# Kernel optimization log

Measured on AMD Instinct MI355X. Metric: run time of the kernel, lower is better.

## Reference

```python
import jax, jax.numpy as jnp
from jax import lax
import numpy as np

EPS = 1e-5  # BatchNorm2d default eps

def _cbs(x, w, g, b, m, v, pad):
    # Conv2d(bias=False) + BatchNorm2d (eval mode, running stats) + SiLU
    y = lax.conv_general_dilated(x, w, (1, 1), [(pad, pad), (pad, pad)],
                                 dimension_numbers=('NCHW', 'OIHW', 'NCHW'))
    y = (y - m[None, :, None, None]) * (g / jnp.sqrt(v + EPS))[None, :, None, None] + b[None, :, None, None]
    return y * jax.nn.sigmoid(y)

def setup_inputs():
    key = jax.random.key(0)
    B, C1, C2, H, W = 2, 128, 128, 20, 20
    ks = iter(jax.random.split(key, 16))
    def wconv(o, i, s):
        return jax.random.normal(next(ks), (o, i, s, s), jnp.float32) / np.float32(np.sqrt(i * s * s))
    def bn(cdim):
        k1, k2 = jax.random.split(next(ks))
        g = jax.random.uniform(k1, (cdim,), jnp.float32, 0.5, 1.5)
        b = jax.random.normal(k2, (cdim,), jnp.float32) * 0.1
        return g, b, jnp.zeros((cdim,), jnp.float32), jnp.ones((cdim,), jnp.float32)
    inp = {'x': jax.random.normal(next(ks), (B, C1, H, W), jnp.float32)}
    inp['w1'] = wconv(C2, C1, 1); inp['g1'], inp['b1'], inp['m1'], inp['v1'] = bn(C2)
    inp['w2'] = wconv(C2, C1, 1); inp['g2'], inp['b2'], inp['m2'], inp['v2'] = bn(C2)
    inp['wr1'] = wconv(C2, 2 * C2, 1); inp['gr1'], inp['br1'], inp['mr1'], inp['vr1'] = bn(C2)
    inp['wr2'] = wconv(C2, C2, 3); inp['gr2'], inp['br2'], inp['mr2'], inp['vr2'] = bn(C2)
    inp['wr3'] = wconv(1, C2, 1); inp['gr3'], inp['br3'], inp['mr3'], inp['vr3'] = bn(1)
    return inp

def reference(x, w1, g1, b1, m1, v1, w2, g2, b2, m2, v2,
              wr1, gr1, br1, mr1, vr1, wr2, gr2, br2, mr2, vr2,
              wr3, gr3, br3, mr3, vr3):
    B, C, H, W = x.shape
    HW = H * W
    # feat: [B, HW, C2]
    feat = _cbs(x, w1, g1, b1, m1, v1, 0).reshape(B, -1, HW).transpose(0, 2, 1)
    C2 = feat.shape[-1]
    # pairwise concat: rel[b,i,j] = [feat[b,i], feat[b,j]]  -> [B, HW, HW, 2*C2]
    fi = jnp.broadcast_to(feat[:, :, None, :], (B, HW, HW, C2))
    fj = jnp.broadcast_to(feat[:, None, :, :], (B, HW, HW, C2))
    rel = jnp.concatenate([fi, fj], axis=-1)
    # faithful permute(0,3,1,2) + contiguous view to [B*HW, 2*C2, H, W]
    rel = rel.transpose(0, 3, 1, 2).reshape(B * HW, 2 * C2, H, W)
    r = _cbs(rel, wr1, gr1, br1, mr1, vr1, 0)
    r = _cbs(r, wr2, gr2, br2, mr2, vr2, 1)
    r = _cbs(r, wr3, gr3, br3, mr3, vr3, 0)  # [B*HW, 1, H, W]
    scores = r.reshape(B, HW, HW)
    # bmm aggregation then back to [B, C2, H, W]
    att = jnp.einsum('bij,bjc->bic', scores, feat).transpose(0, 2, 1).reshape(B, C2, H, W)
    return _cbs(att, w2, g2, b2, m2, v2, 0) + x
```

## Files before the change

### kernel.cpp

```cpp
#include <hip/hip_runtime.h>

#define EPS 1e-5f

typedef __bf16 bf16x8 __attribute__((ext_vector_type(8)));
typedef float  f32x4  __attribute__((ext_vector_type(4)));

__device__ __forceinline__ unsigned short f2bf(float f) {
  unsigned int u = __float_as_uint(f);
  unsigned int r = (u + 0x7fffu + ((u >> 16) & 1u)) >> 16;
  return (unsigned short)r;
}
__device__ __forceinline__ float silu(float y) {
  return y * __builtin_amdgcn_rcpf(1.f + __expf(-y));
}

__global__ void prep_kernel(const float* __restrict__ x, const float* __restrict__ w1,
                            const float* __restrict__ g1, const float* __restrict__ b1,
                            const float* __restrict__ m1, const float* __restrict__ v1,
                            const float* __restrict__ wr2, const float* __restrict__ wr1,
                            float* __restrict__ feat, float* __restrict__ featT,
                            float* __restrict__ attz,
                            unsigned short* __restrict__ Apack, float* __restrict__ Pfx,
                            float* __restrict__ Wt, float* __restrict__ wr1T) {
  int blk = blockIdx.x;
  int tid = threadIdx.x;
  if (blk < 400) {
    int hp = tid >> 7, c = tid & 127;
    int pp = blk * 2 + hp;
    int b = pp / 400, p = pp % 400;
    __shared__ float xv[2][128];
    xv[hp][c] = x[(b * 128 + c) * 400 + p];
    __syncthreads();
    const float4* w4 = (const float4*)(w1 + c * 128);
    const float4* v4 = (const float4*)xv[hp];
    float s0 = 0.f, s1 = 0.f, s2 = 0.f, s3 = 0.f;
#pragma unroll
    for (int i = 0; i < 32; ++i) {
      float4 wv = w4[i], xx = v4[i];
      s0 += wv.x * xx.x; s1 += wv.y * xx.y; s2 += wv.z * xx.z; s3 += wv.w * xx.w;
    }
    float s = (s0 + s1) + (s2 + s3);
    float sc = g1[c] * rsqrtf(v1[c] + EPS);
    float y = s * sc + (b1[c] - m1[c] * sc);
    float f = silu(y);
    feat[(b * 400 + p) * 128 + c] = f;
    featT[(b * 128 + c) * 400 + p] = f;
    if (p >= 200) attz[(b * 400 + p) * 128 + c] = 0.f;
  } else if (blk < 472) {
    int f = (blk - 400) * 4 + (tid >> 6);
    int lane = tid & 63;
    int tap = f >> 5, ks = (f >> 3) & 3, m8 = f & 7;
    int o  = m8 * 16 + (lane & 15);
    int cb = ks * 32 + (lane >> 4) * 8;
    unsigned short* dst = Apack + ((size_t)f * 64 + lane) * 8;
#pragma unroll
    for (int j = 0; j < 8; ++j)
      dst[j] = f2bf(wr2[(o * 128 + (cb + j)) * 9 + tap]);
  } else if (blk < 504) {
    int o = (blk - 472) * 4 + (tid >> 6);
    int lane = tid & 63;
    float4 wv = ((const float4*)(wr1 + o * 256))[lane];
    float p0 = wv.x, p1 = p0 + wv.y, p2 = p1 + wv.z, p3 = p2 + wv.w;
    float v = p3;
#pragma unroll
    for (int d = 1; d < 64; d <<= 1) {
      float t = __shfl_up(v, d);
      if (lane >= d) v += t;
    }
    float off = v - p3;
    float* Po = Pfx + o * 257;
    if (lane == 0) Po[0] = 0.f;
    Po[lane * 4 + 1] = off + p0;
    Po[lane * 4 + 2] = off + p1;
    Po[lane * 4 + 3] = off + p2;
    Po[lane * 4 + 4] = off + p3;
  } else if (blk < 648) {
    int base = (blk - 504) * 1024;
#pragma unroll
    for (int k = 0; k < 4; ++k) {
      int idx = base + k * 256 + tid;
      int tap = idx >> 14;
      int r = idx & 16383;
      int i = r >> 7, o = r & 127;
      Wt[idx] = wr2[(o * 128 + i) * 9 + tap];
    }
  } else {
    int base = (blk - 648) * 1024;
#pragma unroll
    for (int k = 0; k < 4; ++k) {
      int idx = base + k * 256 + tid;
      int i = idx >> 7, o = idx & 127;
      wr1T[idx] = wr1[o * 256 + i];
    }
  }
}

__global__ __launch_bounds__(512, 4) void rel_kernel(
    const float* __restrict__ feat, const float* __restrict__ featT,
    const float* __restrict__ wr1T, const float* __restrict__ Pfx,
    const float* __restrict__ gr1, const float* __restrict__ br1,
    const float* __restrict__ mr1, const float* __restrict__ vr1,
    const unsigned short* __restrict__ Apack, const float* __restrict__ Wt,
    const float* __restrict__ gr2, const float* __restrict__ br2,
    const float* __restrict__ mr2, const float* __restrict__ vr2,
    const float* __restrict__ wr3,
    const float* __restrict__ gr3, const float* __restrict__ br3,
    const float* __restrict__ mr3, const float* __restrict__ vr3,
    float* __restrict__ att) {

  __shared__ __align__(16) unsigned short r1f[16 * 221 * 8];
  __shared__ float f0s[220], f1s[220], scoreS[208];
  __shared__ float wB0s[128], wB1s[128];
  __shared__ float sc1[128], sh1[128], sc2[128], sh2[128], w3c[128];
  __shared__ float attT[128];
  __shared__ float fA[256], r1c[128], AvS[128];
  __shared__ float vS[9 * 128];
  __shared__ float spS[9];
  __shared__ float spP[400];

  int tid = threadIdx.x, lane = tid & 63, wid = tid >> 6;
  int blk = blockIdx.x;

  if (tid < 128) {
    float s1 = gr1[tid] * rsqrtf(vr1[tid] + EPS); sc1[tid] = s1; sh1[tid] = br1[tid] - mr1[tid] * s1;
    float s2 = gr2[tid] * rsqrtf(vr2[tid] + EPS); sc2[tid] = s2; sh2[tid] = br2[tid] - mr2[tid] * s2;
    w3c[tid] = wr3[tid];
    attT[tid] = 0.f; AvS[tid] = 0.f;
  }
  float s3 = gr3[0] * rsqrtf(vr3[0] + EPS);
  float sh3 = br3[0] - mr3[0] * s3;

  if (blk < 800) {
    int idx = blk >> 1, half = blk & 1;
    int b = idx / 200, q = 200 + idx % 200;
    int c0 = (q * 256) / 400, c1 = c0 + 1;
    if (tid < 128) {
      const float* Po = Pfx + tid * 257;
      int e0 = min(256, 400 * c0 + 400 - 256 * q);
      wB0s[tid] = Po[e0];
      float wv = 0.f;
      if (c1 < 256) {
        int s1i = min(256, max(0, 400 * c1 - 256 * q));
        wv = Po[256] - Po[s1i];
      }
      wB1s[tid] = wv;
    }
    if (tid < 220) {
      int p = tid + 180 * half;
      f0s[tid] = featT[(b * 128 + (c0 - 128)) * 400 + p];
      f1s[tid] = (c1 < 256) ? featT[(b * 128 + (c1 - 128)) * 400 + p] : 0.f;
    }
    if (tid < 208) scoreS[tid] = 0.f;
    __syncthreads();

    for (int i = tid; i < 3520; i += 512) {
      int plane = i / 220, p = i - plane * 220;
      int cb = (plane >> 2) * 32 + (plane & 3) * 8;
      float fa0 = f0s[p], fa1 = f1s[p];
      unsigned int pk[4];
#pragma unroll
      for (int jp = 0; jp < 4; ++jp) {
        int c = cb + jp * 2;
        float y0 = wB0s[c] * fa0 + wB1s[c] * fa1;     y0 = y0 * sc1[c] + sh1[c];
        float y1 = wB0s[c + 1] * fa0 + wB1s[c + 1] * fa1; y1 = y1 * sc1[c + 1] + sh1[c + 1];
        pk[jp] = (unsigned int)f2bf(silu(y0)) | ((unsigned int)f2bf(silu(y1)) << 16);
      }
      *(uint4*)&r1f[(plane * 221 + p) * 8] = make_uint4(pk[0], pk[1], pk[2], pk[3]);
    }
    if (tid < 16) *(uint4*)&r1f[(tid * 221 + 220) * 8] = make_uint4(0, 0, 0, 0);

    int wm = wid & 1, wn = wid >> 1;
    int ntcnt = (wn == 0) ? 4 : 3;
    int n16 = lane & 15, quad = lane >> 4;
    int hA[4], wA[4], poA[4]; bool pov[4];
#pragma unroll
    for (int t = 0; t < 4; ++t) {
      int po = (wn + 4 * t) * 16 + n16;
      poA[t] = po; pov[t] = po < 200;
      int pg = half * 200 + po;
      hA[t] = pg / 20; wA[t] = pg - 20 * hA[t];
    }
    f32x4 acc[4][4];
#pragma unroll
    for (int mt = 0; mt < 4; ++mt)
#pragma unroll
      for (int t = 0; t < 4; ++t) acc[mt][t] = f32x4{0.f, 0.f, 0.f, 0.f};

    __syncthreads();

    const char* wbase = (const char*)Apack + (size_t)((wm * 4) * 64 + lane) * 16;
    for (int tap = 0; tap < 9; ++tap) {
      int dy = tap / 3 - 1, dx = tap % 3 - 1;
      int pp[4];
#pragma unroll
      for (int t = 0; t < 4; ++t) {
        int hh = hA[t] + dy, ww = wA[t] + dx;
        bool valid = pov[t] & (hh >= 0) & (hh < 20) & (ww >= 0) & (ww < 20);
        pp[t] = valid ? (hh - 9 * half) * 20 + ww : 220;
      }
#pragma unroll
      for (int ks = 0; ks < 4; ++ks) {
        const char* wp = wbase + (size_t)(tap * 4 + ks) * 8192;
        bf16x8 af0 = *(const bf16x8*)(wp);
        bf16x8 af1 = *(const bf16x8*)(wp + 1024);
        bf16x8 af2 = *(const bf16x8*)(wp + 2048);
        bf16x8 af3 = *(const bf16x8*)(wp + 3072);
        int pbase = (ks * 4 + quad) * 221;
#pragma unroll
        for (int t = 0; t < 4; ++t) {
          if (t < ntcnt) {
            bf16x8 bfr = *(const bf16x8*)&r1f[(pbase + pp[t]) * 8];
            acc[0][t] = __builtin_amdgcn_mfma_f32_16x16x32_bf16(af0, bfr, acc[0][t], 0, 0, 0);
            acc[1][t] = __builtin_amdgcn_mfma_f32_16x16x32_bf16(af1, bfr, acc[1][t], 0, 0, 0);
            acc[2][t] = __builtin_amdgcn_mfma_f32_16x16x32_bf16(af2, bfr, acc[2][t], 0, 0, 0);
            acc[3][t] = __builtin_amdgcn_mfma_f32_16x16x32_bf16(af3, bfr, acc[3][t], 0, 0, 0);
          }
        }
      }
    }

#pragma unroll
    for (int t = 0; t < 4; ++t) {
      if (t < ntcnt) {
        float ps = 0.f;
#pragma unroll
        for (int mt = 0; mt < 4; ++mt) {
#pragma unroll
          for (int r = 0; r < 4; ++r) {
            int o = wm * 64 + mt * 16 + quad * 4 + r;
            float y = acc[mt][t][r] * sc2[o] + sh2[o];
            ps += silu(y) * w3c[o];
          }
        }
        ps += __shfl_xor(ps, 16);
        ps += __shfl_xor(ps, 32);
        if (quad == 0 && pov[t]) atomicAdd(&scoreS[poA[t]], ps);
      }
    }
    __syncthreads();

    if (tid < 200) scoreS[tid] = silu(scoreS[tid] * s3 + sh3);
    __syncthreads();

    {
      int c = tid & 127, part = tid >> 7;
      float s = 0.f;
      int j0 = part * 50;
      const float* fb = feat + ((size_t)(b * 400 + half * 200 + j0)) * 128 + c;
#pragma unroll 10
      for (int j = 0; j < 50; ++j)
        s += scoreS[j0 + j] * fb[(size_t)j * 128];
      atomicAdd(&attT[c], s);
    }
    __syncthreads();
    if (tid < 128)
      atomicAdd(&att[((size_t)(b * 400 + q)) * 128 + tid], attT[tid]);
  } else {
    int cidx = blk - 800;
    int b = cidx / 200, q = cidx % 200;
    if (tid < 256) {
      int u = q * 256 + tid; int c = u / 400, i2 = u - c * 400;
      fA[tid] = featT[(b * 128 + c) * 400 + i2];
    }
    for (int k = tid; k < 1152; k += 512) vS[k] = 0.f;
    __syncthreads();
    {
      int o = tid & 127, part = tid >> 7;
      const float* wt = wr1T + part * 64 * 128 + o;
      const float* fv = fA + part * 64;
      float a = 0.f;
#pragma unroll 8
      for (int k = 0; k < 64; ++k) a += wt[k * 128] * fv[k];
      atomicAdd(&AvS[o], a);
    }
    __syncthreads();
    if (tid < 128) r1c[tid] = silu(AvS[tid] * sc1[tid] + sh1[tid]);
    __syncthreads();
    {
      int o = tid & 127, part = tid >> 7;
      const float* rc = r1c + part * 32;
      for (int tap = 0; tap < 9; ++tap) {
        const float* wt = Wt + tap * 16384 + part * 32 * 128 + o;
        float s = 0.f;
#pragma unroll 8
        for (int i2 = 0; i2 < 32; ++i2) s += wt[i2 * 128] * rc[i2];
        atomicAdd(&vS[tap * 128 + o], s);
      }
    }
    __syncthreads();
    for (int pat = wid; pat < 9; pat += 8) {
      int ry = pat / 3, rx = pat % 3;
      float ps = 0.f;
      for (int oo = lane; oo < 128; oo += 64) {
        float y = 0.f;
#pragma unroll
        for (int dy = -1; dy <= 1; ++dy) {
          if ((ry == 0 && dy < 0) || (ry == 2 && dy > 0)) continue;
#pragma unroll
          for (int dx = -1; dx <= 1; ++dx) {
            if ((rx == 0 && dx < 0) || (rx == 2 && dx > 0)) continue;
            y += vS[((dy + 1) * 3 + (dx + 1)) * 128 + oo];
          }
        }
        y = y * sc2[oo] + sh2[oo];
        ps += silu(y) * w3c[oo];
      }
#pragma unroll
      for (int sft = 32; sft >= 1; sft >>= 1) ps += __shfl_xor(ps, sft);
      if (lane == 0) spS[pat] = silu(ps * s3 + sh3);
    }
    __syncthreads();

    for (int p = tid; p < 400; p += 512) {
      int r = p / 20, cm = p - 20 * r;
      int ry = (r == 0) ? 0 : (r == 19) ? 2 : 1;
      int rx = (cm == 0) ? 0 : (cm == 19) ? 2 : 1;
      spP[p] = spS[ry * 3 + rx];
    }
    __syncthreads();
    {
      int c = tid & 127, part = tid >> 7;
      const float* fb = feat + ((size_t)(b * 400) + part * 100) * 128 + c;
      const float* sp = spP + part * 100;
      float s = 0.f;
#pragma unroll 10
      for (int j = 0; j < 100; ++j) s += sp[j] * fb[(size_t)j * 128];
      atomicAdd(&attT[c], s);
    }
    __syncthreads();
    if (tid < 128)
      att[((size_t)(b * 400 + q)) * 128 + tid] = attT[tid];
  }
}

__global__ void out_kernel(const float* __restrict__ att, const float* __restrict__ x,
                           const float* __restrict__ w2,
                           const float* __restrict__ g2, const float* __restrict__ b2,
                           const float* __restrict__ m2, const float* __restrict__ v2,
                           float* __restrict__ out) {
  int pp = blockIdx.x;
  int b = pp / 400, p = pp % 400;
  int tid = threadIdx.x;
  __shared__ float av[128];
  if (tid < 128) av[tid] = att[(size_t)(b * 400 + p) * 128 + tid];
  __syncthreads();
  int c = tid >> 1, part = tid & 1;
  const float4* w4 = (const float4*)(w2 + c * 128 + part * 64);
  const float4* v4 = (const float4*)(av + part * 64);
  float s0 = 0.f, s1 = 0.f, s2 = 0.f, s3 = 0.f;
#pragma unroll
  for (int i = 0; i < 16; ++i) {
    float4 wv = w4[i], xx = v4[i];
    s0 += wv.x * xx.x; s1 += wv.y * xx.y; s2 += wv.z * xx.z; s3 += wv.w * xx.w;
  }
  float s = (s0 + s1) + (s2 + s3);
  s += __shfl_xor(s, 1);
  if (part == 0) {
    float sc = g2[c] * rsqrtf(v2[c] + EPS);
    float y = s * sc + (b2[c] - m2[c] * sc);
    int xi = (b * 128 + c) * 400 + p;
    out[xi] = silu(y) + x[xi];
  }
}

extern "C" void kernel_launch(void* const* d_in, const int* in_sizes, int n_in,
                              void* d_out, int out_size, void* d_ws, size_t ws_size,
                              hipStream_t stream) {
  const float* x   = (const float*)d_in[0];
  const float* w1  = (const float*)d_in[1];
  const float* g1  = (const float*)d_in[2];
  const float* b1  = (const float*)d_in[3];
  const float* m1  = (const float*)d_in[4];
  const float* v1  = (const float*)d_in[5];
  const float* w2  = (const float*)d_in[6];
  const float* g2  = (const float*)d_in[7];
  const float* b2  = (const float*)d_in[8];
  const float* m2  = (const float*)d_in[9];
  const float* v2  = (const float*)d_in[10];
  const float* wr1 = (const float*)d_in[11];
  const float* gr1 = (const float*)d_in[12];
  const float* br1 = (const float*)d_in[13];
  const float* mr1 = (const float*)d_in[14];
  const float* vr1 = (const float*)d_in[15];
  const float* wr2 = (const float*)d_in[16];
  const float* gr2 = (const float*)d_in[17];
  const float* br2 = (const float*)d_in[18];
  const float* mr2 = (const float*)d_in[19];
  const float* vr2 = (const float*)d_in[20];
  const float* wr3 = (const float*)d_in[21];
  const float* gr3 = (const float*)d_in[22];
  const float* br3 = (const float*)d_in[23];
  const float* mr3 = (const float*)d_in[24];
  const float* vr3 = (const float*)d_in[25];
  float* out = (float*)d_out;

  char* ws = (char*)d_ws;
  float*          feat  = (float*)ws;
  float*          attb  = (float*)(ws + 409600);
  unsigned short* Apack = (unsigned short*)(ws + 819200);
  float*          Pfx   = (float*)(ws + 1114112);
  float*          Wt    = (float*)(ws + 1245696);
  float*          featT = (float*)(ws + 1901056);
  float*          wr1T  = (float*)(ws + 2310656);

  prep_kernel<<<680, 256, 0, stream>>>(x, w1, g1, b1, m1, v1, wr2, wr1,
                                       feat, featT, attb, Apack, Pfx, Wt, wr1T);
  rel_kernel<<<1200, 512, 0, stream>>>(feat, featT, wr1T, Pfx, gr1, br1, mr1, vr1,
                                       Apack, Wt,
                                       gr2, br2, mr2, vr2, wr3, gr3, br3, mr3, vr3, attb);
  out_kernel<<<800, 256, 0, stream>>>(attb, x, w2, g2, b2, m2, v2, out);
}
```

Measured before the change: 205.2 us.

## Fuse output conv into rel kernel using last-block completion counters

Drops the separate out_kernel. The final 1x1 conv, BN, SiLU and residual add now run inside rel_kernel. For the pair-split rows, a per-row atomic counter (zeroed in prep_kernel) picks the second finishing block, which reads the accumulated att row and writes the output. The single-block rows compute the output straight from shared memory. This removes one kernel launch and a global round-trip of att, at the cost of a threadfence, an extra atomic and a serialized tail in some blocks. The counter buffer reuses workspace rows that are no longer written.

```diff
diff --git a/kernel.cpp b/kernel.cpp
--- a/kernel.cpp
+++ b/kernel.cpp
@@ -19,7 +19,7 @@
                             const float* __restrict__ m1, const float* __restrict__ v1,
                             const float* __restrict__ wr2, const float* __restrict__ wr1,
                             float* __restrict__ feat, float* __restrict__ featT,
-                            float* __restrict__ attz,
+                            float* __restrict__ attz, int* __restrict__ cnt,
                             unsigned short* __restrict__ Apack, float* __restrict__ Pfx,
                             float* __restrict__ Wt, float* __restrict__ wr1T) {
   int blk = blockIdx.x;
@@ -45,7 +45,10 @@
     float f = silu(y);
     feat[(b * 400 + p) * 128 + c] = f;
     featT[(b * 128 + c) * 400 + p] = f;
-    if (p >= 200) attz[(b * 400 + p) * 128 + c] = 0.f;
+    if (p >= 200) {
+      attz[(b * 400 + p) * 128 + c] = 0.f;
+      if (c == 0) cnt[b * 200 + (p - 200)] = 0;
+    }
   } else if (blk < 472) {
     int f = (blk - 400) * 4 + (tid >> 6);
     int lane = tid & 63;
@@ -106,17 +109,23 @@
     const float* __restrict__ wr3,
     const float* __restrict__ gr3, const float* __restrict__ br3,
     const float* __restrict__ mr3, const float* __restrict__ vr3,
-    float* __restrict__ att) {
+    float* __restrict__ att, int* __restrict__ cnt,
+    const float* __restrict__ x, const float* __restrict__ w2,
+    const float* __restrict__ g2, const float* __restrict__ b2,
+    const float* __restrict__ m2, const float* __restrict__ v2,
+    float* __restrict__ out) {
 
   __shared__ __align__(16) unsigned short r1f[16 * 221 * 8];
   __shared__ float f0s[220], f1s[220], scoreS[208];
   __shared__ float wB0s[128], wB1s[128];
   __shared__ float sc1[128], sh1[128], sc2[128], sh2[128], w3c[128];
-  __shared__ float attT[128];
-  __shared__ float fA[256], r1c[128], AvS[128];
+  __shared__ __align__(16) float attT[128];
+  __shared__ __align__(16) float fA[256];
+  __shared__ float r1c[128], AvS[128];
   __shared__ float vS[9 * 128];
   __shared__ float spS[9];
   __shared__ float spP[400];
+  __shared__ int lastFlag;
 
   int tid = threadIdx.x, lane = tid & 63, wid = tid >> 6;
   int blk = blockIdx.x;
@@ -255,6 +264,34 @@
     __syncthreads();
     if (tid < 128)
       atomicAdd(&att[((size_t)(b * 400 + q)) * 128 + tid], attT[tid]);
+    __threadfence();
+    __syncthreads();
+    if (tid == 0)
+      lastFlag = (atomicAdd(&cnt[b * 200 + (q - 200)], 1) == 1);
+    __syncthreads();
+    if (lastFlag) {
+      float* arow = att + ((size_t)(b * 400 + q)) * 128;
+      if (tid < 128) fA[tid] = atomicAdd(&arow[tid], 0.0f);
+      __syncthreads();
+      int c = tid >> 2, sub = tid & 3;
+      const float4* w4 = (const float4*)(w2 + c * 128 + sub * 32);
+      const float4* v4 = (const float4*)(fA + sub * 32);
+      float s0 = 0.f, s1 = 0.f, s2v = 0.f, s3v = 0.f;
+#pragma unroll
+      for (int i = 0; i < 8; ++i) {
+        float4 wv = w4[i], xx = v4[i];
+        s0 += wv.x * xx.x; s1 += wv.y * xx.y; s2v += wv.z * xx.z; s3v += wv.w * xx.w;
+      }
+      float s = (s0 + s1) + (s2v + s3v);
+      s += __shfl_xor(s, 1);
+      s += __shfl_xor(s, 2);
+      if (sub == 0) {
+        float scc = g2[c] * rsqrtf(v2[c] + EPS);
+        float y = s * scc + (b2[c] - m2[c] * scc);
+        int xi = (b * 128 + c) * 400 + q;
+        out[xi] = silu(y) + x[xi];
+      }
+    }
   } else {
     int cidx = blk - 800;
     int b = cidx / 200, q = cidx % 200;
@@ -328,38 +365,26 @@
       atomicAdd(&attT[c], s);
     }
     __syncthreads();
-    if (tid < 128)
-      att[((size_t)(b * 400 + q)) * 128 + tid] = attT[tid];
-  }
-}
-
-__global__ void out_kernel(const float* __restrict__ att, const float* __restrict__ x,
-                           const float* __restrict__ w2,
-                           const float* __restrict__ g2, const float* __restrict__ b2,
-                           const float* __restrict__ m2, const float* __restrict__ v2,
-                           float* __restrict__ out) {
-  int pp = blockIdx.x;
-  int b = pp / 400, p = pp % 400;
-  int tid = threadIdx.x;
-  __shared__ float av[128];
-  if (tid < 128) av[tid] = att[(size_t)(b * 400 + p) * 128 + tid];
-  __syncthreads();
-  int c = tid >> 1, part = tid & 1;
-  const float4* w4 = (const float4*)(w2 + c * 128 + part * 64);
-  const float4* v4 = (const float4*)(av + part * 64);
-  float s0 = 0.f, s1 = 0.f, s2 = 0.f, s3 = 0.f;
-#pragma unroll
-  for (int i = 0; i < 16; ++i) {
-    float4 wv = w4[i], xx = v4[i];
-    s0 += wv.x * xx.x; s1 += wv.y * xx.y; s2 += wv.z * xx.z; s3 += wv.w * xx.w;
-  }
-  float s = (s0 + s1) + (s2 + s3);
-  s += __shfl_xor(s, 1);
-  if (part == 0) {
-    float sc = g2[c] * rsqrtf(v2[c] + EPS);
-    float y = s * sc + (b2[c] - m2[c] * sc);
-    int xi = (b * 128 + c) * 400 + p;
-    out[xi] = silu(y) + x[xi];
+    {
+      int c = tid >> 2, sub = tid & 3;
+      const float4* w4 = (const float4*)(w2 + c * 128 + sub * 32);
+      const float4* v4 = (const float4*)(attT + sub * 32);
+      float s0 = 0.f, s1 = 0.f, s2v = 0.f, s3v = 0.f;
+#pragma unroll
+      for (int i = 0; i < 8; ++i) {
+        float4 wv = w4[i], xx = v4[i];
+        s0 += wv.x * xx.x; s1 += wv.y * xx.y; s2v += wv.z * xx.z; s3v += wv.w * xx.w;
+      }
+      float s = (s0 + s1) + (s2v + s3v);
+      s += __shfl_xor(s, 1);
+      s += __shfl_xor(s, 2);
+      if (sub == 0) {
+        float scc = g2[c] * rsqrtf(v2[c] + EPS);
+        float y = s * scc + (b2[c] - m2[c] * scc);
+        int xi = (b * 128 + c) * 400 + q;
+        out[xi] = silu(y) + x[xi];
+      }
+    }
   }
 }
 
@@ -397,6 +422,7 @@
   char* ws = (char*)d_ws;
   float*          feat  = (float*)ws;
   float*          attb  = (float*)(ws + 409600);
+  int*            cnt   = (int*)(ws + 409600);
   unsigned short* Apack = (unsigned short*)(ws + 819200);
   float*          Pfx   = (float*)(ws + 1114112);
   float*          Wt    = (float*)(ws + 1245696);
@@ -404,9 +430,9 @@
   float*          wr1T  = (float*)(ws + 2310656);
 
   prep_kernel<<<680, 256, 0, stream>>>(x, w1, g1, b1, m1, v1, wr2, wr1,
-                                       feat, featT, attb, Apack, Pfx, Wt, wr1T);
+                                       feat, featT, attb, cnt, Apack, Pfx, Wt, wr1T);
   rel_kernel<<<1200, 512, 0, stream>>>(feat, featT, wr1T, Pfx, gr1, br1, mr1, vr1,
                                        Apack, Wt,
-                                       gr2, br2, mr2, vr2, wr3, gr3, br3, mr3, vr3, attb);
-  out_kernel<<<800, 256, 0, stream>>>(attb, x, w2, g2, b2, m2, v2, out);
+                                       gr2, br2, mr2, vr2, wr3, gr3, br3, mr3, vr3,
+                                       attb, cnt, x, w2, g2, b2, m2, v2, out);
 }
```

Measured after the change: 292.1 us. 42.4% more time.
